# Kernel optimization log

Hardware: AMD Instinct MI355X
Metric: run time of the kernel (lower is better)

## Reference

```python
import jax, jax.numpy as jnp
import numpy as np

DIM, HID, E, K = 1024, 2048, 8, 2


def setup_inputs() -> dict:
    key = jax.random.key(0)
    ks = jax.random.split(key, 5)
    x = jax.random.normal(ks[0], (2, 2048, DIM), dtype=jnp.float32)
    # router (torch zero-inits; use small random so routing is non-degenerate)
    router_w = jax.random.normal(ks[1], (DIM, E), dtype=jnp.float32) * 0.02
    router_b = jnp.zeros((E,), dtype=jnp.float32)
    # stacked expert params: w12 [E, dim, 2*hidden], w3 [E, hidden, dim]
    w12 = jax.random.normal(ks[2], (E, DIM, 2 * HID), dtype=jnp.float32) * 0.02
    w3 = jax.random.normal(ks[3], (E, HID, DIM), dtype=jnp.float32) * 0.02
    return {"x": x, "router_w": router_w, "router_b": router_b, "w12": w12, "w3": w3}


def reference(x, router_w, router_b, w12, w3):
    # router logits [b, s, e]; eval mode -> no jitter noise
    logits = jnp.einsum("bsd,de->bse", x, router_w) + router_b
    scores = jax.nn.sigmoid(logits)
    top_v, top_i = jax.lax.top_k(scores, K)            # [b, s, k]
    rw = top_v / (jnp.sum(top_v, axis=-1, keepdims=True) + 1e-6)
    # per-token combine weight for each expert (0 if not routed)
    oh = jax.nn.one_hot(top_i, E, dtype=x.dtype)       # [b, s, k, e]
    cw = jnp.einsum("bsk,bske->bse", rw, oh)           # [b, s, e]
    # dense all-expert SwiGLU (matches original masked-dense math)
    x12 = jnp.einsum("bsd,edh->bseh", x, w12)          # [b, s, e, 2H]
    x1, x2 = jnp.split(x12, 2, axis=-1)
    h = jax.nn.silu(x1) * x2                           # [b, s, e, H]
    eout = jnp.einsum("bseh,ehd->bsed", h, w3)         # [b, s, e, dim]
    out = jnp.einsum("bsed,bse->bsd", eout, cw)
    aux_loss = 0.01 * jnp.mean(logits ** 2)
    return out, aux_loss
```

## Files before the change

### kernel.cpp

```cpp
#include <hip/hip_runtime.h>
#include <hip/hip_bf16.h>
#include <stdint.h>

typedef __bf16 bf16_t;
typedef __bf16 bf16x8 __attribute__((ext_vector_type(8)));
typedef __bf16 bf16x4 __attribute__((ext_vector_type(4)));
typedef float f32x4 __attribute__((ext_vector_type(4)));
typedef uint32_t u32x2 __attribute__((ext_vector_type(2)));
typedef __attribute__((address_space(3))) const uint8_t* lds3;

#define T_TOK 4096
#define DIM   1024
#define HID   2048
#define NE    8
#define MAXT  72

__device__ __forceinline__ void gload_lds16(const void* g, void* l) {
  __builtin_amdgcn_global_load_lds(
      (const __attribute__((address_space(1))) unsigned int*)g,
      (__attribute__((address_space(3))) unsigned int*)l, 16, 0, 0);
}

#define TRR(dst, a, OFF) \
  asm volatile("ds_read_b64_tr_b16 %0, %1 offset:" OFF : "=v"(dst) : "v"(a))

__device__ __forceinline__ bf16x8 mk8(u32x2 lo, u32x2 hi) {
  uint4 t; t.x = lo[0]; t.y = lo[1]; t.z = hi[0]; t.w = hi[1];
  return __builtin_bit_cast(bf16x8, t);
}

__global__ __launch_bounds__(256) void k_conv(const float* __restrict__ w12,
    const float* __restrict__ w3, bf16_t* __restrict__ w12c, bf16_t* __restrict__ w3c) {
  const size_t N12 = 33554432ull;
  const size_t NT  = 50331648ull;
  const size_t stride = (size_t)gridDim.x * 256 * 4;
  for (size_t i = ((size_t)blockIdx.x * 256 + threadIdx.x) * 4; i < NT; i += stride) {
    if (i < N12) {
      float4 v = *(const float4*)(w12 + i);
      bf16x4 o; o[0]=(bf16_t)v.x; o[1]=(bf16_t)v.y; o[2]=(bf16_t)v.z; o[3]=(bf16_t)v.w;
      *(bf16x4*)(w12c + i) = o;
    } else {
      size_t j = i - N12;
      float4 v = *(const float4*)(w3 + j);
      bf16x4 o; o[0]=(bf16_t)v.x; o[1]=(bf16_t)v.y; o[2]=(bf16_t)v.z; o[3]=(bf16_t)v.w;
      *(bf16x4*)(w3c + j) = o;
    }
  }
}

__global__ __launch_bounds__(256) void k_router(const float* __restrict__ x,
    const float* __restrict__ rw, const float* __restrict__ rb,
    int* __restrict__ counts, int* __restrict__ top_i, float* __restrict__ top_w,
    float* __restrict__ aux, bf16_t* __restrict__ xb) {
  int t = blockIdx.x * 4 + (threadIdx.x >> 6);
  int lane = threadIdx.x & 63;
  const float* xt = x + (size_t)t * DIM;
  float acc[8] = {0.f,0.f,0.f,0.f,0.f,0.f,0.f,0.f};
#pragma unroll
  for (int it = 0; it < 4; ++it) {
    int i = (it * 64 + lane) * 4;
    float4 xv = *(const float4*)(xt + i);
    bf16x4 o;
    o[0] = (bf16_t)xv.x; o[1] = (bf16_t)xv.y; o[2] = (bf16_t)xv.z; o[3] = (bf16_t)xv.w;
    *(bf16x4*)(xb + (size_t)t * DIM + i) = o;
#pragma unroll
    for (int c = 0; c < 4; ++c) {
      float v = (c == 0) ? xv.x : (c == 1) ? xv.y : (c == 2) ? xv.z : xv.w;
      float4 r0 = *(const float4*)(rw + (size_t)(i + c) * 8);
      float4 r1 = *(const float4*)(rw + (size_t)(i + c) * 8 + 4);
      acc[0] += v * r0.x; acc[1] += v * r0.y; acc[2] += v * r0.z; acc[3] += v * r0.w;
      acc[4] += v * r1.x; acc[5] += v * r1.y; acc[6] += v * r1.z; acc[7] += v * r1.w;
    }
  }
#pragma unroll
  for (int m = 32; m >= 1; m >>= 1) {
#pragma unroll
    for (int e = 0; e < 8; ++e) acc[e] += __shfl_xor(acc[e], m, 64);
  }
  if (lane == 0) {
    float s[8]; float sumsq = 0.f;
#pragma unroll
    for (int e = 0; e < 8; ++e) {
      float lg = acc[e] + rb[e];
      sumsq += lg * lg;
      s[e] = 1.f / (1.f + __expf(-lg));
    }
    int i1 = 0;
#pragma unroll
    for (int e = 1; e < 8; ++e) if (s[e] > s[i1]) i1 = e;
    int i2 = (i1 == 0) ? 1 : 0;
#pragma unroll
    for (int e = 0; e < 8; ++e) if (e != i1 && s[e] > s[i2]) i2 = e;
    float v1 = s[i1], v2 = s[i2];
    float den = v1 + v2 + 1e-6f;
    top_i[2 * t]     = i1; top_i[2 * t + 1] = i2;
    top_w[2 * t]     = v1 / den;
    top_w[2 * t + 1] = v2 / den;
    atomicAdd(&counts[i1], 1);
    atomicAdd(&counts[i2], 1);
    atomicAdd(aux, 0.01f * sumsq * (1.f / 32768.f));
  }
}

__global__ void k_plan(const int* __restrict__ counts, int* __restrict__ base,
                       int* __restrict__ tile_e, int* __restrict__ tile_m0) {
  if (threadIdx.x == 0) {
    int s = 0, nt = 0;
    for (int e = 0; e < NE; ++e) {
      base[e] = s;
      int c = counts[e];
      for (int m0 = 0; m0 < c; m0 += 128) { tile_e[nt] = e; tile_m0[nt] = m0; ++nt; }
      s += c;
    }
    for (; nt < MAXT; ++nt) tile_e[nt] = -1;
  }
}

__global__ __launch_bounds__(256) void k_gather(const int* __restrict__ top_i,
    const float* __restrict__ top_w, const int* __restrict__ base,
    int* __restrict__ fill, int* __restrict__ slot_token, float* __restrict__ slot_wt,
    int* __restrict__ slot_of) {
  int t = blockIdx.x * 256 + threadIdx.x;
  if (t >= T_TOK) return;
#pragma unroll
  for (int j = 0; j < 2; ++j) {
    int e = top_i[2 * t + j];
    int p = atomicAdd(&fill[e], 1);
    int g = base[e] + p;
    slot_token[g] = t;
    slot_wt[g]    = top_w[2 * t + j];
    slot_of[2 * t + j] = g;
  }
}

__global__ __launch_bounds__(256) void k_gemm1(
    const bf16_t* __restrict__ xb, const bf16_t* __restrict__ w12c,
    const int* __restrict__ counts, const int* __restrict__ base,
    const int* __restrict__ tile_e, const int* __restrict__ tile_m0,
    const int* __restrict__ slot_token, bf16_t* __restrict__ h) {
  const int e = tile_e[blockIdx.y];
  if (e < 0) return;
  const int m0  = tile_m0[blockIdx.y];
  const int cnt = counts[e];
  const int bas = base[e];
  const int n0  = blockIdx.x * 64;
  const bf16_t* W1 = w12c + (size_t)e * (1024u * 4096u) + n0;
  const bf16_t* W2 = W1 + 2048;

  __shared__ bf16_t sA[2][128 * 64];
  __shared__ bf16_t sB1[2][64 * 64];
  __shared__ bf16_t sB2[2][64 * 64];

  const int tid = threadIdx.x, lane = tid & 63, wid = tid >> 6;
  const int wr = wid >> 1, wc = wid & 1;
  const int lr = lane >> 3, sw = (lane & 7) ^ lr;

  int tokA[4];
#pragma unroll
  for (int i = 0; i < 4; ++i) {
    int row = m0 + wid * 32 + i * 8 + lr;
    tokA[i] = slot_token[bas + (row < cnt ? row : cnt - 1)];
  }

  int brow0, bcol0, brow1, bcol1;
  { int b = tid >> 3, w = tid & 7;
    brow0 = ((b >> 2) << 2) + (w >> 1); bcol0 = (b & 3) * 16 + (w & 1) * 8; }
  { int g2 = 256 + tid; int b = g2 >> 3, w = g2 & 7;
    brow1 = ((b >> 2) << 2) + (w >> 1); bcol1 = (b & 3) * 16 + (w & 1) * 8; }

  auto stage = [&](int p, int k0) {
#pragma unroll
    for (int i = 0; i < 4; ++i)
      gload_lds16(xb + (size_t)tokA[i] * DIM + k0 + sw * 8,
                  &sA[p][(wid * 32 + i * 8) * 64]);
    gload_lds16(W1 + (size_t)(k0 + brow0) * 4096 + bcol0, &sB1[p][tid * 8]);
    gload_lds16(W1 + (size_t)(k0 + brow1) * 4096 + bcol1, &sB1[p][2048 + tid * 8]);
    gload_lds16(W2 + (size_t)(k0 + brow0) * 4096 + bcol0, &sB2[p][tid * 8]);
    gload_lds16(W2 + (size_t)(k0 + brow1) * 4096 + bcol1, &sB2[p][2048 + tid * 8]);
  };

  const int trOff = (lane >> 4) * 1024 + wc * 256 + (lane & 15) * 8;
  lds3 bB1 = (lds3)(const uint8_t*)&sB1[0][0];
  lds3 bB2 = (lds3)(const uint8_t*)&sB2[0][0];

  f32x4 acc1[4][2] = {};
  f32x4 acc2[4][2] = {};

  stage(0, 0);
  stage(1, 64);

  const int NT = DIM / 64;
  for (int t = 0; t < NT; ++t) {
    const int p = t & 1;
    if (t + 2 < NT) asm volatile("s_waitcnt vmcnt(8)" ::: "memory");
    else            asm volatile("s_waitcnt vmcnt(0)" ::: "memory");
    __builtin_amdgcn_s_barrier();
    asm volatile("" ::: "memory");
    __builtin_amdgcn_s_setprio(1);
#pragma unroll
    for (int kk = 0; kk < 2; ++kk) {
      const int g = kk * 4 + (lane >> 4);
      bf16x8 a[4];
#pragma unroll
      for (int mf = 0; mf < 4; ++mf) {
        int r = wr * 64 + mf * 16 + (lane & 15);
        a[mf] = *(const bf16x8*)(&sA[p][r * 64 + ((g ^ (r & 7)) << 3)]);
      }
      lds3 a1 = bB1 + p * 8192 + kk * 4096 + trOff;
      lds3 a2 = bB2 + p * 8192 + kk * 4096 + trOff;
      u32x2 q0, q1, q2, q3, s0, s1, s2, s3;
      TRR(q0, a1, "0");   TRR(q1, a1, "512");
      TRR(q2, a1, "128"); TRR(q3, a1, "640");
      TRR(s0, a2, "0");   TRR(s1, a2, "512");
      TRR(s2, a2, "128"); TRR(s3, a2, "640");
      asm volatile("s_waitcnt lgkmcnt(0)" ::: "memory");
      __builtin_amdgcn_sched_barrier(0);
      bf16x8 b1f[2] = { mk8(q0, q1), mk8(q2, q3) };
      bf16x8 b2f[2] = { mk8(s0, s1), mk8(s2, s3) };
#pragma unroll
      for (int mf = 0; mf < 4; ++mf)
#pragma unroll
        for (int nf = 0; nf < 2; ++nf) {
          acc1[mf][nf] = __builtin_amdgcn_mfma_f32_16x16x32_bf16(a[mf], b1f[nf], acc1[mf][nf], 0, 0, 0);
          acc2[mf][nf] = __builtin_amdgcn_mfma_f32_16x16x32_bf16(a[mf], b2f[nf], acc2[mf][nf], 0, 0, 0);
        }
    }
    __builtin_amdgcn_s_setprio(0);
    __builtin_amdgcn_sched_barrier(0);
    __builtin_amdgcn_s_barrier();
    asm volatile("" ::: "memory");
    if (t + 2 < NT) stage(p, (t + 2) * 64);
  }

#pragma unroll
  for (int mf = 0; mf < 4; ++mf)
#pragma unroll
    for (int r = 0; r < 4; ++r) {
      int m = wr * 64 + mf * 16 + ((lane >> 4) << 2) + r;
      if (m0 + m < cnt) {
        size_t rowoff = (size_t)(bas + m0 + m) * HID + n0;
#pragma unroll
        for (int nf = 0; nf < 2; ++nf) {
          int col = wc * 32 + nf * 16 + (lane & 15);
          float d1 = acc1[mf][nf][r], d2 = acc2[mf][nf][r];
          h[rowoff + col] = (bf16_t)((d1 / (1.f + __expf(-d1))) * d2);
        }
      }
    }
}

__global__ __launch_bounds__(256) void k_gemm2(
    const bf16_t* __restrict__ h, const bf16_t* __restrict__ w3c,
    const int* __restrict__ counts, const int* __restrict__ base,
    const int* __restrict__ tile_e, const int* __restrict__ tile_m0,
    const float* __restrict__ slot_wt, bf16_t* __restrict__ eout) {
  const int e = tile_e[blockIdx.y];
  if (e < 0) return;
  const int m0  = tile_m0[blockIdx.y];
  const int cnt = counts[e];
  const int bas = base[e];
  const int n0 = blockIdx.x * 128;
  const bf16_t* W = w3c + (size_t)e * (2048u * 1024u) + n0;

  __shared__ bf16_t sA[2][128 * 64];
  __shared__ bf16_t sB[2][128 * 64];

  const int tid = threadIdx.x, lane = tid & 63, wid = tid >> 6;
  const int wr = wid >> 1, wc = wid & 1;
  const int lr = lane >> 3, sw = (lane & 7) ^ lr;

  int rowA[4];
#pragma unroll
  for (int i = 0; i < 4; ++i) {
    int row = m0 + wid * 32 + i * 8 + lr;
    rowA[i] = bas + (row < cnt ? row : cnt - 1);
  }

  int br[4], bc[4];
#pragma unroll
  for (int j = 0; j < 4; ++j) {
    int g = j * 256 + tid;
    int b = g >> 3, w = g & 7;
    br[j] = ((b >> 3) << 2) + (w >> 1);
    bc[j] = (b & 7) * 16 + (w & 1) * 8;
  }

  auto stage = [&](int p, int k0) {
#pragma unroll
    for (int i = 0; i < 4; ++i)
      gload_lds16(h + (size_t)rowA[i] * HID + k0 + sw * 8,
                  &sA[p][(wid * 32 + i * 8) * 64]);
#pragma unroll
    for (int j = 0; j < 4; ++j)
      gload_lds16(W + (size_t)(k0 + br[j]) * 1024 + bc[j],
                  &sB[p][(j * 256 + tid) * 8]);
  };

  const int trOff = (lane >> 4) * 2048 + wc * 512 + (lane & 15) * 8;
  lds3 bB = (lds3)(const uint8_t*)&sB[0][0];

  f32x4 acc[4][4] = {};

  stage(0, 0);
  stage(1, 64);

  const int NT = HID / 64;
  for (int t = 0; t < NT; ++t) {
    const int p = t & 1;
    if (t + 2 < NT) asm volatile("s_waitcnt vmcnt(8)" ::: "memory");
    else            asm volatile("s_waitcnt vmcnt(0)" ::: "memory");
    __builtin_amdgcn_s_barrier();
    asm volatile("" ::: "memory");
    __builtin_amdgcn_s_setprio(1);
#pragma unroll
    for (int kk = 0; kk < 2; ++kk) {
      const int g = kk * 4 + (lane >> 4);
      bf16x8 a[4];
#pragma unroll
      for (int mf = 0; mf < 4; ++mf) {
        int r = wr * 64 + mf * 16 + (lane & 15);
        a[mf] = *(const bf16x8*)(&sA[p][r * 64 + ((g ^ (r & 7)) << 3)]);
      }
      lds3 ab = bB + p * 16384 + kk * 8192 + trOff;
      u32x2 q0, q1, q2, q3, q4, q5, q6, q7;
      TRR(q0, ab, "0");   TRR(q1, ab, "1024");
      TRR(q2, ab, "128"); TRR(q3, ab, "1152");
      TRR(q4, ab, "256"); TRR(q5, ab, "1280");
      TRR(q6, ab, "384"); TRR(q7, ab, "1408");
      asm volatile("s_waitcnt lgkmcnt(0)" ::: "memory");
      __builtin_amdgcn_sched_barrier(0);
      bf16x8 bf[4] = { mk8(q0, q1), mk8(q2, q3), mk8(q4, q5), mk8(q6, q7) };
#pragma unroll
      for (int mf = 0; mf < 4; ++mf)
#pragma unroll
        for (int nf = 0; nf < 4; ++nf)
          acc[mf][nf] = __builtin_amdgcn_mfma_f32_16x16x32_bf16(a[mf], bf[nf], acc[mf][nf], 0, 0, 0);
    }
    __builtin_amdgcn_s_setprio(0);
    __builtin_amdgcn_sched_barrier(0);
    __builtin_amdgcn_s_barrier();
    asm volatile("" ::: "memory");
    if (t + 2 < NT) stage(p, (t + 2) * 64);
  }

#pragma unroll
  for (int mf = 0; mf < 4; ++mf)
#pragma unroll
    for (int r = 0; r < 4; ++r) {
      int m = wr * 64 + mf * 16 + ((lane >> 4) << 2) + r;
      if (m0 + m < cnt) {
        int gs = bas + m0 + m;
        float wt = slot_wt[gs];
        size_t o = (size_t)gs * DIM + n0;
#pragma unroll
        for (int nf = 0; nf < 4; ++nf) {
          int col = wc * 64 + nf * 16 + (lane & 15);
          eout[o + col] = (bf16_t)(acc[mf][nf][r] * wt);
        }
      }
    }
}

__global__ __launch_bounds__(256) void k_combine(const bf16_t* __restrict__ eout,
    const int* __restrict__ slot_of, float* __restrict__ out) {
  const int t = blockIdx.x;
  const int c = threadIdx.x * 4;
  const int g0 = slot_of[2 * t], g1 = slot_of[2 * t + 1];
  bf16x4 a = *(const bf16x4*)(eout + (size_t)g0 * DIM + c);
  bf16x4 b = *(const bf16x4*)(eout + (size_t)g1 * DIM + c);
  float4 o;
  o.x = (float)a[0] + (float)b[0];
  o.y = (float)a[1] + (float)b[1];
  o.z = (float)a[2] + (float)b[2];
  o.w = (float)a[3] + (float)b[3];
  *(float4*)(out + (size_t)t * DIM + c) = o;
}

extern "C" void kernel_launch(void* const* d_in, const int* in_sizes, int n_in,
                              void* d_out, int out_size, void* d_ws, size_t ws_size,
                              hipStream_t stream) {
  const float* x   = (const float*)d_in[0];
  const float* rw  = (const float*)d_in[1];
  const float* rb  = (const float*)d_in[2];
  const float* w12 = (const float*)d_in[3];
  const float* w3  = (const float*)d_in[4];
  float* out = (float*)d_out;
  float* aux = out + (size_t)T_TOK * DIM;

  char* ws = (char*)d_ws;
  int*   counts     = (int*)(ws + 0);
  int*   fill       = (int*)(ws + 64);
  int*   base       = (int*)(ws + 128);
  int*   top_i      = (int*)(ws + 4096);
  float* top_w      = (float*)(ws + 4096 + 32768);
  int*   slot_token = (int*)(ws + 4096 + 65536);
  float* slot_wt    = (float*)(ws + 4096 + 98304);
  int*   slot_of    = (int*)(ws + 4096 + 131072);
  int*   tile_e     = (int*)(ws + 4096 + 163840);
  int*   tile_m0    = (int*)(ws + 4096 + 164352);
  bf16_t* xb        = (bf16_t*)(ws + 262144);
  bf16_t* h         = (bf16_t*)(ws + 262144 + 8388608);
  bf16_t* w12c      = (bf16_t*)(ws + 262144 + 8388608 + 33554432);
  bf16_t* w3c       = (bf16_t*)((char*)w12c + 67108864);
  bf16_t* eout      = w12c;

  hipMemsetAsync(ws, 0, 256, stream);
  hipMemsetAsync(aux, 0, sizeof(float), stream);

  k_conv<<<dim3(2048), dim3(256), 0, stream>>>(w12, w3, w12c, w3c);
  k_router<<<dim3(T_TOK / 4), dim3(256), 0, stream>>>(x, rw, rb, counts, top_i, top_w,
                                                      aux, xb);
  k_plan<<<dim3(1), dim3(64), 0, stream>>>(counts, base, tile_e, tile_m0);
  k_gather<<<dim3(T_TOK / 256), dim3(256), 0, stream>>>(top_i, top_w, base, fill,
                                                        slot_token, slot_wt, slot_of);
  k_gemm1<<<dim3(HID / 64, MAXT), dim3(256), 0, stream>>>(
      xb, w12c, counts, base, tile_e, tile_m0, slot_token, h);
  k_gemm2<<<dim3(DIM / 128, MAXT), dim3(256), 0, stream>>>(
      h, w3c, counts, base, tile_e, tile_m0, slot_wt, eout);
  k_combine<<<dim3(T_TOK), dim3(256), 0, stream>>>(eout, slot_of, out);
}
```

Baseline: 386.0 us.

## Fuse fp32-to-bf16 weight conversion into grouped GEMM B-tile loads

Removes the separate k_conv pass that converted all expert weights to bf16 in workspace. The two GEMM kernels now read fp32 weights into registers, convert them, and write bf16 into a single-buffered LDS tile each k-step. The aim is to drop a full 400MB read-and-write pass over the weights. In exchange the pipeline becomes register-prefetch plus synchronous LDS writes. Each weight tile is also now read as fp32 (twice the bytes) by every m-tile block of the same expert.

```diff
diff --git a/kernel.cpp b/kernel.cpp
--- a/kernel.cpp
+++ b/kernel.cpp
@@ -29,23 +29,9 @@
   return __builtin_bit_cast(bf16x8, t);
 }
 
-__global__ __launch_bounds__(256) void k_conv(const float* __restrict__ w12,
-    const float* __restrict__ w3, bf16_t* __restrict__ w12c, bf16_t* __restrict__ w3c) {
-  const size_t N12 = 33554432ull;
-  const size_t NT  = 50331648ull;
-  const size_t stride = (size_t)gridDim.x * 256 * 4;
-  for (size_t i = ((size_t)blockIdx.x * 256 + threadIdx.x) * 4; i < NT; i += stride) {
-    if (i < N12) {
-      float4 v = *(const float4*)(w12 + i);
-      bf16x4 o; o[0]=(bf16_t)v.x; o[1]=(bf16_t)v.y; o[2]=(bf16_t)v.z; o[3]=(bf16_t)v.w;
-      *(bf16x4*)(w12c + i) = o;
-    } else {
-      size_t j = i - N12;
-      float4 v = *(const float4*)(w3 + j);
-      bf16x4 o; o[0]=(bf16_t)v.x; o[1]=(bf16_t)v.y; o[2]=(bf16_t)v.z; o[3]=(bf16_t)v.w;
-      *(bf16x4*)(w3c + j) = o;
-    }
-  }
+__device__ __forceinline__ bf16x4 cvt4(float4 v) {
+  bf16x4 o; o[0] = (bf16_t)v.x; o[1] = (bf16_t)v.y; o[2] = (bf16_t)v.z; o[3] = (bf16_t)v.w;
+  return o;
 }
 
 __global__ __launch_bounds__(256) void k_router(const float* __restrict__ x,
@@ -60,9 +46,7 @@
   for (int it = 0; it < 4; ++it) {
     int i = (it * 64 + lane) * 4;
     float4 xv = *(const float4*)(xt + i);
-    bf16x4 o;
-    o[0] = (bf16_t)xv.x; o[1] = (bf16_t)xv.y; o[2] = (bf16_t)xv.z; o[3] = (bf16_t)xv.w;
-    *(bf16x4*)(xb + (size_t)t * DIM + i) = o;
+    *(bf16x4*)(xb + (size_t)t * DIM + i) = cvt4(xv);
 #pragma unroll
     for (int c = 0; c < 4; ++c) {
       float v = (c == 0) ? xv.x : (c == 1) ? xv.y : (c == 2) ? xv.z : xv.w;
@@ -134,7 +118,7 @@
 }
 
 __global__ __launch_bounds__(256) void k_gemm1(
-    const bf16_t* __restrict__ xb, const bf16_t* __restrict__ w12c,
+    const bf16_t* __restrict__ xb, const float* __restrict__ w12,
     const int* __restrict__ counts, const int* __restrict__ base,
     const int* __restrict__ tile_e, const int* __restrict__ tile_m0,
     const int* __restrict__ slot_token, bf16_t* __restrict__ h) {
@@ -144,12 +128,12 @@
   const int cnt = counts[e];
   const int bas = base[e];
   const int n0  = blockIdx.x * 64;
-  const bf16_t* W1 = w12c + (size_t)e * (1024u * 4096u) + n0;
-  const bf16_t* W2 = W1 + 2048;
+  const float* Wf1 = w12 + (size_t)e * (1024u * 4096u) + n0;
+  const float* Wf2 = Wf1 + 2048;
 
   __shared__ bf16_t sA[2][128 * 64];
-  __shared__ bf16_t sB1[2][64 * 64];
-  __shared__ bf16_t sB2[2][64 * 64];
+  __shared__ bf16_t sB1[64 * 64];
+  __shared__ bf16_t sB2[64 * 64];
 
   const int tid = threadIdx.x, lane = tid & 63, wid = tid >> 6;
   const int wr = wid >> 1, wc = wid & 1;
@@ -162,40 +146,52 @@
     tokA[i] = slot_token[bas + (row < cnt ? row : cnt - 1)];
   }
 
-  int brow0, bcol0, brow1, bcol1;
-  { int b = tid >> 3, w = tid & 7;
-    brow0 = ((b >> 2) << 2) + (w >> 1); bcol0 = (b & 3) * 16 + (w & 1) * 8; }
-  { int g2 = 256 + tid; int b = g2 >> 3, w = g2 & 7;
-    brow1 = ((b >> 2) << 2) + (w >> 1); bcol1 = (b & 3) * 16 + (w & 1) * 8; }
-
-  auto stage = [&](int p, int k0) {
+  const int krow = tid >> 4;
+  const int n4l  = (tid & 15) * 4;
+  const int wB = (krow >> 2) * 512 + (krow & 3) * 32
+               + (n4l >> 4) * 128 + ((n4l >> 3) & 1) * 16 + (n4l & 7) * 2;
+
+  float4 b1r[4], b2r[4];
+
+  auto issueA = [&](int p, int k0) {
 #pragma unroll
     for (int i = 0; i < 4; ++i)
       gload_lds16(xb + (size_t)tokA[i] * DIM + k0 + sw * 8,
                   &sA[p][(wid * 32 + i * 8) * 64]);
-    gload_lds16(W1 + (size_t)(k0 + brow0) * 4096 + bcol0, &sB1[p][tid * 8]);
-    gload_lds16(W1 + (size_t)(k0 + brow1) * 4096 + bcol1, &sB1[p][2048 + tid * 8]);
-    gload_lds16(W2 + (size_t)(k0 + brow0) * 4096 + bcol0, &sB2[p][tid * 8]);
-    gload_lds16(W2 + (size_t)(k0 + brow1) * 4096 + bcol1, &sB2[p][2048 + tid * 8]);
+  };
+  auto issueB = [&](int k0) {
+#pragma unroll
+    for (int i = 0; i < 4; ++i) {
+      size_t row = (size_t)(k0 + i * 16 + krow) * 4096 + n4l;
+      b1r[i] = *(const float4*)(Wf1 + row);
+      b2r[i] = *(const float4*)(Wf2 + row);
+    }
+  };
+  auto writeB = [&]() {
+    char* c1 = (char*)sB1, *c2 = (char*)sB2;
+#pragma unroll
+    for (int i = 0; i < 4; ++i) {
+      *(bf16x4*)(c1 + i * 2048 + wB) = cvt4(b1r[i]);
+      *(bf16x4*)(c2 + i * 2048 + wB) = cvt4(b2r[i]);
+    }
   };
 
   const int trOff = (lane >> 4) * 1024 + wc * 256 + (lane & 15) * 8;
-  lds3 bB1 = (lds3)(const uint8_t*)&sB1[0][0];
-  lds3 bB2 = (lds3)(const uint8_t*)&sB2[0][0];
+  lds3 bB1 = (lds3)(const uint8_t*)sB1;
+  lds3 bB2 = (lds3)(const uint8_t*)sB2;
 
   f32x4 acc1[4][2] = {};
   f32x4 acc2[4][2] = {};
 
-  stage(0, 0);
-  stage(1, 64);
+  issueA(0, 0); issueB(0);
 
   const int NT = DIM / 64;
   for (int t = 0; t < NT; ++t) {
     const int p = t & 1;
-    if (t + 2 < NT) asm volatile("s_waitcnt vmcnt(8)" ::: "memory");
-    else            asm volatile("s_waitcnt vmcnt(0)" ::: "memory");
-    __builtin_amdgcn_s_barrier();
-    asm volatile("" ::: "memory");
+    asm volatile("s_waitcnt vmcnt(0)" ::: "memory");
+    writeB();
+    __syncthreads();
+    if (t + 1 < NT) { issueA(p ^ 1, (t + 1) * 64); issueB((t + 1) * 64); }
     __builtin_amdgcn_s_setprio(1);
 #pragma unroll
     for (int kk = 0; kk < 2; ++kk) {
@@ -206,8 +202,8 @@
         int r = wr * 64 + mf * 16 + (lane & 15);
         a[mf] = *(const bf16x8*)(&sA[p][r * 64 + ((g ^ (r & 7)) << 3)]);
       }
-      lds3 a1 = bB1 + p * 8192 + kk * 4096 + trOff;
-      lds3 a2 = bB2 + p * 8192 + kk * 4096 + trOff;
+      lds3 a1 = bB1 + kk * 4096 + trOff;
+      lds3 a2 = bB2 + kk * 4096 + trOff;
       u32x2 q0, q1, q2, q3, s0, s1, s2, s3;
       TRR(q0, a1, "0");   TRR(q1, a1, "512");
       TRR(q2, a1, "128"); TRR(q3, a1, "640");
@@ -227,9 +223,7 @@
     }
     __builtin_amdgcn_s_setprio(0);
     __builtin_amdgcn_sched_barrier(0);
-    __builtin_amdgcn_s_barrier();
-    asm volatile("" ::: "memory");
-    if (t + 2 < NT) stage(p, (t + 2) * 64);
+    __syncthreads();
   }
 
 #pragma unroll
@@ -250,7 +244,7 @@
 }
 
 __global__ __launch_bounds__(256) void k_gemm2(
-    const bf16_t* __restrict__ h, const bf16_t* __restrict__ w3c,
+    const bf16_t* __restrict__ h, const float* __restrict__ w3,
     const int* __restrict__ counts, const int* __restrict__ base,
     const int* __restrict__ tile_e, const int* __restrict__ tile_m0,
     const float* __restrict__ slot_wt, bf16_t* __restrict__ eout) {
@@ -260,10 +254,10 @@
   const int cnt = counts[e];
   const int bas = base[e];
   const int n0 = blockIdx.x * 128;
-  const bf16_t* W = w3c + (size_t)e * (2048u * 1024u) + n0;
+  const float* Wf = w3 + (size_t)e * (2048u * 1024u) + n0;
 
   __shared__ bf16_t sA[2][128 * 64];
-  __shared__ bf16_t sB[2][128 * 64];
+  __shared__ bf16_t sB[128 * 64];
 
   const int tid = threadIdx.x, lane = tid & 63, wid = tid >> 6;
   const int wr = wid >> 1, wc = wid & 1;
@@ -276,41 +270,45 @@
     rowA[i] = bas + (row < cnt ? row : cnt - 1);
   }
 
-  int br[4], bc[4];
-#pragma unroll
-  for (int j = 0; j < 4; ++j) {
-    int g = j * 256 + tid;
-    int b = g >> 3, w = g & 7;
-    br[j] = ((b >> 3) << 2) + (w >> 1);
-    bc[j] = (b & 7) * 16 + (w & 1) * 8;
-  }
-
-  auto stage = [&](int p, int k0) {
+  const int krow2 = tid >> 5;
+  const int n4l2  = (tid & 31) * 4;
+  const int wB2 = (krow2 >> 2) * 1024 + (krow2 & 3) * 32
+                + (n4l2 >> 4) * 128 + ((n4l2 >> 3) & 1) * 16 + (n4l2 & 7) * 2;
+
+  float4 br[8];
+
+  auto issueA = [&](int p, int k0) {
 #pragma unroll
     for (int i = 0; i < 4; ++i)
       gload_lds16(h + (size_t)rowA[i] * HID + k0 + sw * 8,
                   &sA[p][(wid * 32 + i * 8) * 64]);
-#pragma unroll
-    for (int j = 0; j < 4; ++j)
-      gload_lds16(W + (size_t)(k0 + br[j]) * 1024 + bc[j],
-                  &sB[p][(j * 256 + tid) * 8]);
+  };
+  auto issueB = [&](int k0) {
+#pragma unroll
+    for (int i = 0; i < 8; ++i)
+      br[i] = *(const float4*)(Wf + (size_t)(k0 + i * 8 + krow2) * 1024 + n4l2);
+  };
+  auto writeB = [&]() {
+    char* c = (char*)sB;
+#pragma unroll
+    for (int i = 0; i < 8; ++i)
+      *(bf16x4*)(c + i * 2048 + wB2) = cvt4(br[i]);
   };
 
   const int trOff = (lane >> 4) * 2048 + wc * 512 + (lane & 15) * 8;
-  lds3 bB = (lds3)(const uint8_t*)&sB[0][0];
+  lds3 bB = (lds3)(const uint8_t*)sB;
 
   f32x4 acc[4][4] = {};
 
-  stage(0, 0);
-  stage(1, 64);
+  issueA(0, 0); issueB(0);
 
   const int NT = HID / 64;
   for (int t = 0; t < NT; ++t) {
     const int p = t & 1;
-    if (t + 2 < NT) asm volatile("s_waitcnt vmcnt(8)" ::: "memory");
-    else            asm volatile("s_waitcnt vmcnt(0)" ::: "memory");
-    __builtin_amdgcn_s_barrier();
-    asm volatile("" ::: "memory");
+    asm volatile("s_waitcnt vmcnt(0)" ::: "memory");
+    writeB();
+    __syncthreads();
+    if (t + 1 < NT) { issueA(p ^ 1, (t + 1) * 64); issueB((t + 1) * 64); }
     __builtin_amdgcn_s_setprio(1);
 #pragma unroll
     for (int kk = 0; kk < 2; ++kk) {
@@ -321,7 +319,7 @@
         int r = wr * 64 + mf * 16 + (lane & 15);
         a[mf] = *(const bf16x8*)(&sA[p][r * 64 + ((g ^ (r & 7)) << 3)]);
       }
-      lds3 ab = bB + p * 16384 + kk * 8192 + trOff;
+      lds3 ab = bB + kk * 8192 + trOff;
       u32x2 q0, q1, q2, q3, q4, q5, q6, q7;
       TRR(q0, ab, "0");   TRR(q1, ab, "1024");
       TRR(q2, ab, "128"); TRR(q3, ab, "1152");
@@ -338,9 +336,7 @@
     }
     __builtin_amdgcn_s_setprio(0);
     __builtin_amdgcn_sched_barrier(0);
-    __builtin_amdgcn_s_barrier();
-    asm volatile("" ::: "memory");
-    if (t + 2 < NT) stage(p, (t + 2) * 64);
+    __syncthreads();
   }
 
 #pragma unroll
@@ -400,22 +396,19 @@
   int*   tile_m0    = (int*)(ws + 4096 + 164352);
   bf16_t* xb        = (bf16_t*)(ws + 262144);
   bf16_t* h         = (bf16_t*)(ws + 262144 + 8388608);
-  bf16_t* w12c      = (bf16_t*)(ws + 262144 + 8388608 + 33554432);
-  bf16_t* w3c       = (bf16_t*)((char*)w12c + 67108864);
-  bf16_t* eout      = w12c;
+  bf16_t* eout      = (bf16_t*)(ws + 262144 + 8388608 + 33554432);
 
   hipMemsetAsync(ws, 0, 256, stream);
   hipMemsetAsync(aux, 0, sizeof(float), stream);
 
-  k_conv<<<dim3(2048), dim3(256), 0, stream>>>(w12, w3, w12c, w3c);
   k_router<<<dim3(T_TOK / 4), dim3(256), 0, stream>>>(x, rw, rb, counts, top_i, top_w,
                                                       aux, xb);
   k_plan<<<dim3(1), dim3(64), 0, stream>>>(counts, base, tile_e, tile_m0);
   k_gather<<<dim3(T_TOK / 256), dim3(256), 0, stream>>>(top_i, top_w, base, fill,
                                                         slot_token, slot_wt, slot_of);
   k_gemm1<<<dim3(HID / 64, MAXT), dim3(256), 0, stream>>>(
-      xb, w12c, counts, base, tile_e, tile_m0, slot_token, h);
+      xb, w12, counts, base, tile_e, tile_m0, slot_token, h);
   k_gemm2<<<dim3(DIM / 128, MAXT), dim3(256), 0, stream>>>(
-      h, w3c, counts, base, tile_e, tile_m0, slot_wt, eout);
+      h, w3, counts, base, tile_e, tile_m0, slot_wt, eout);
   k_combine<<<dim3(T_TOK), dim3(256), 0, stream>>>(eout, slot_of, out);
 }
```

Result: slower. 438.3 us (+13.6%).
